# Optimization experiments

Hardware: AMD Instinct MI355X
Metric: run time of the kernel (lower is better)

Reference implementation:

```python
import jax, jax.numpy as jnp
import numpy as np

N_NODES = 50000
N_PATHS = 4
N_EDGES = 800000
D_IN = 256
D_OUT = 256
D_HID = 128  # SemanticAttention default hidden_size


def setup_inputs() -> dict:
    key = jax.random.key(0)
    ks = jax.random.split(key, 6)
    x = jax.random.normal(ks[0], (N_NODES, D_IN), dtype=jnp.float32)
    edge_indices = jax.random.randint(ks[1], (N_PATHS, 2, N_EDGES), 0, N_NODES)
    Ws = jax.random.normal(ks[2], (N_PATHS, D_IN, D_OUT), dtype=jnp.float32) * (1.0 / np.sqrt(D_IN))
    bs = jnp.zeros((N_PATHS, D_OUT), dtype=jnp.float32)
    attn_w1 = jax.random.normal(ks[3], (D_OUT, D_HID), dtype=jnp.float32) * (1.0 / np.sqrt(D_OUT))
    attn_b1 = jnp.zeros((D_HID,), dtype=jnp.float32)
    attn_w2 = jax.random.normal(ks[4], (D_HID, 1), dtype=jnp.float32) * (1.0 / np.sqrt(D_HID))
    return {"x": x, "edge_indices": edge_indices, "Ws": Ws, "bs": bs,
            "attn_w1": attn_w1, "attn_b1": attn_b1, "attn_w2": attn_w2}


def _gcn_conv(x, W, b, edges):
    """PyG GCNConv with normalize=True, add_self_loops=True.
    out = D^{-1/2} (A + I) D^{-1/2} (x @ W) + b
    """
    n = x.shape[0]
    xw = x @ W  # [N, D_OUT]
    loop = jnp.arange(n, dtype=edges.dtype)
    src = jnp.concatenate([edges[0], loop])
    dst = jnp.concatenate([edges[1], loop])
    ones = jnp.ones(src.shape[0], dtype=x.dtype)
    deg = jax.ops.segment_sum(ones, dst, num_segments=n)  # in-degree incl. self loop
    dinv = jnp.where(deg > 0, jax.lax.rsqrt(deg), 0.0)
    norm = dinv[src] * dinv[dst]  # [E+N]
    msgs = xw[src] * norm[:, None]  # gather + scale
    return jax.ops.segment_sum(msgs, dst, num_segments=n) + b  # scatter-add


def reference(x, edge_indices, Ws, bs, attn_w1, attn_b1, attn_w2):
    P = edge_indices.shape[0]
    # per-meta-path GCN embeddings, stacked -> [N, P, D_OUT]
    z = jnp.stack([_gcn_conv(x, Ws[i], bs[i], edge_indices[i]) for i in range(P)], axis=1)
    # semantic attention: per-node softmax over meta-paths
    w = jnp.tanh(z @ attn_w1 + attn_b1) @ attn_w2  # [N, P, 1]
    beta = jax.nn.softmax(w, axis=1)
    return (beta * z).sum(axis=1)  # [N, D_OUT]
```

## Files before the change

### kernel.cpp

```cpp
#include <hip/hip_runtime.h>
#include <hip/hip_fp16.h>
#include <cstdint>
#include <cstddef>

#define NN 50000
#define NE 800000
#define NP 4
#define DD 256
#define HH 128
#define MPAD 50048
#define PADIDX 50000
#define NCH 8

#define NB 196
#define CAP 5120
#define SCAP 6144
#define EPB 4096
#define NBB ((NE + EPB - 1) / EPB)
#define BIN_BLOCKS (NBB * NP)

typedef _Float16 f16x8 __attribute__((ext_vector_type(8)));
typedef float f32x4 __attribute__((ext_vector_type(4)));
typedef unsigned short u16x8 __attribute__((ext_vector_type(8)));

#define X_OCT (NN * DD / 8)
#define XP_OCT (MPAD * DD / 8)
#define W_OCT (NP * DD * DD / 8)
#define W1_OCT (HH * DD / 8)
#define CVT_BLOCKS ((XP_OCT + W_OCT + W1_OCT + 255) / 256)
#define AGG_BLOCKS (NCH * NP * (MPAD / 64))
#define GEMM_BLOCKS ((MPAD / 64) * NP)
#define AT_BLOCKS ((NN + 31) / 32)

__global__ __launch_bounds__(256) void k_bin(const int* __restrict__ edges,
                                             int* __restrict__ gcnt,
                                             unsigned int* __restrict__ binned,
                                             const float* __restrict__ x,
                                             const float* __restrict__ Ws,
                                             const float* __restrict__ w1,
                                             _Float16* __restrict__ xhc,
                                             _Float16* __restrict__ Wt,
                                             _Float16* __restrict__ w1t) {
    const int bx = blockIdx.x;
    const int tid = threadIdx.x;
    if (bx < BIN_BLOCKS) {
        __shared__ int hist[256], lb[256], cur[256], gbase[256], wsum[4];
        __shared__ unsigned int stage[EPB];
        const int p  = bx / NBB;
        const int bc = bx - p * NBB;
        const int e0 = bc * EPB;
        const int total = min(EPB, NE - e0);
        const int* es = edges + (size_t)p * 2 * NE;
        const int* ed = es + NE;
        hist[tid] = 0;
        __syncthreads();
        unsigned int word[16];
        int bkt[16];
#pragma unroll
        for (int j = 0; j < 16; j++) {
            int e = e0 + j * 256 + tid;
            bkt[j] = -1;
            if (e < NE) {
                int dst = ed[e];
                int src = es[e];
                int b = dst >> 8;
                bkt[j] = b;
                word[j] = ((unsigned)b << 24) | ((unsigned)(dst & 255) << 16) | (unsigned)src;
                atomicAdd(&hist[b], 1);
            }
        }
        __syncthreads();
        const int lane = tid & 63, wv = tid >> 6;
        int v = hist[tid];
        int incl = v;
#pragma unroll
        for (int off = 1; off < 64; off <<= 1) {
            int u = __shfl_up(incl, off);
            if (lane >= off) incl += u;
        }
        if (lane == 63) wsum[wv] = incl;
        __syncthreads();
        int wbase = 0;
        for (int i = 0; i < wv; i++) wbase += wsum[i];
        int excl = wbase + incl - v;
        lb[tid] = excl;
        cur[tid] = excl;
        if (tid < NB && v > 0) gbase[tid] = atomicAdd(&gcnt[p * NB + tid], v);
        __syncthreads();
#pragma unroll
        for (int j = 0; j < 16; j++)
            if (bkt[j] >= 0) {
                int r = atomicAdd(&cur[bkt[j]], 1);
                stage[r] = word[j];
            }
        __syncthreads();
        for (int s = tid; s < total; s += 256) {
            unsigned int wd = stage[s];
            int b = wd >> 24;
            int posl = gbase[b] + (s - lb[b]);
            if (posl < CAP)
                binned[(size_t)(p * NB + b) * CAP + posl] = wd & 0x00FFFFFFu;
        }
        return;
    }
    int i = (bx - BIN_BLOCKS) * 256 + tid;
    if (i < XP_OCT) {
        f16x8 o;
        if (i < X_OCT) {
            const float4* src = (const float4*)x + (size_t)i * 2;
            float4 v0 = src[0], v1 = src[1];
            o[0] = (_Float16)v0.x; o[1] = (_Float16)v0.y; o[2] = (_Float16)v0.z; o[3] = (_Float16)v0.w;
            o[4] = (_Float16)v1.x; o[5] = (_Float16)v1.y; o[6] = (_Float16)v1.z; o[7] = (_Float16)v1.w;
        } else {
#pragma unroll
            for (int t = 0; t < 8; t++) o[t] = (_Float16)0.0f;
        }
        int row = i >> 5, oc = i & 31;
        int c = oc >> 2, q = oc & 3;
        *(f16x8*)(xhc + ((size_t)c * MPAD + row) * 32 + q * 8) = o;
    } else if (i < XP_OCT + W_OCT) {
        int j = i - XP_OCT;
        int p   = j / (DD * DD / 8);
        int rem = j - p * (DD * DD / 8);
        int n   = rem >> 5;
        int k8  = (rem & 31) * 8;
        const float* wp = Ws + (size_t)p * DD * DD;
        f16x8 o;
#pragma unroll
        for (int t = 0; t < 8; t++) o[t] = (_Float16)wp[(size_t)(k8 + t) * DD + n];
        *((f16x8*)(Wt + (size_t)p * DD * DD + (size_t)n * DD + k8)) = o;
    } else if (i < XP_OCT + W_OCT + W1_OCT) {
        int j = i - XP_OCT - W_OCT;
        int n  = j >> 5;
        int k8 = (j & 31) * 8;
        f16x8 o;
#pragma unroll
        for (int t = 0; t < 8; t++) o[t] = (_Float16)w1[(size_t)(k8 + t) * HH + n];
        *((f16x8*)(w1t + (size_t)n * DD + k8)) = o;
    }
}

__global__ __launch_bounds__(256) void k_sort(const int* __restrict__ gcnt,
                                              const unsigned int* __restrict__ binned,
                                              unsigned short* __restrict__ srcs,
                                              int* __restrict__ offs,
                                              int* __restrict__ ends,
                                              float* __restrict__ dinv) {
    __shared__ int hist[256], cur[256], wsum[4];
    __shared__ unsigned short sorted[SCAP];
    const int bx = blockIdx.x;
    const int tid = threadIdx.x;
    const int p = bx / NB, b = bx - p * NB;
    const int base = bx * SCAP;
    const int n = min(gcnt[bx], CAP);
    hist[tid] = 0;
#pragma unroll
    for (int j = 0; j < SCAP / 256; j++) sorted[j * 256 + tid] = (unsigned short)PADIDX;
    __syncthreads();
    unsigned int w[20];
#pragma unroll
    for (int j = 0; j < 20; j++) {
        int s = j * 256 + tid;
        w[j] = 0xFFFFFFFFu;
        if (s < n) {
            w[j] = binned[(size_t)bx * CAP + s];
            atomicAdd(&hist[(w[j] >> 16) & 255], 1);
        }
    }
    __syncthreads();
    const int lane = tid & 63, wv = tid >> 6;
    int v  = hist[tid];
    int pv = (v + 7) & ~7;
    int incl = pv;
#pragma unroll
    for (int off = 1; off < 64; off <<= 1) {
        int u = __shfl_up(incl, off);
        if (lane >= off) incl += u;
    }
    if (lane == 63) wsum[wv] = incl;
    __syncthreads();
    int wbase = 0;
    for (int i = 0; i < wv; i++) wbase += wsum[i];
    int excl = wbase + incl - pv;
    cur[tid] = excl;
    const int node = b * 256 + tid;
    if (node < NN) {
        int o = base + excl;
        offs[p * NN + node] = o;
        ends[p * NN + node] = o + pv;
        dinv[(size_t)p * MPAD + node] = rsqrtf((float)v + 1.0f);
    }
    __syncthreads();
    int totalpad = wsum[0] + wsum[1] + wsum[2] + wsum[3];
#pragma unroll
    for (int j = 0; j < 20; j++)
        if (w[j] != 0xFFFFFFFFu) {
            int r = atomicAdd(&cur[(w[j] >> 16) & 255], 1);
            if (r < SCAP) sorted[r] = (unsigned short)(w[j] & 0xFFFFu);
        }
    __syncthreads();
#pragma unroll
    for (int j = 0; j < SCAP / 256; j++) {
        int s = j * 256 + tid;
        if (s < totalpad && s < SCAP) srcs[base + s] = sorted[s];
    }
}

__global__ __launch_bounds__(256) void k_agg(const _Float16* __restrict__ xhc,
                                             const float* __restrict__ dinv,
                                             const int* __restrict__ offs,
                                             const int* __restrict__ ends,
                                             const unsigned short* __restrict__ srcs,
                                             _Float16* __restrict__ aggc) {
    const int c  = blockIdx.x & 7;
    const int r  = blockIdx.x >> 3;
    const int p  = r / (MPAD / 64);
    const int nb = r - p * (MPAD / 64);
    const int wv = threadIdx.x >> 6;
    const int lane = threadIdx.x & 63;
    const int g = lane >> 2;
    const int f = lane & 3;
    const int n = nb * 64 + wv * 16 + g;

    const _Float16* xc = xhc + (size_t)c * MPAD * 32 + f * 8;
    const float* dvp = dinv + (size_t)p * MPAD;
    const float dd = dvp[n];

    float facc[8];
    {
        f16x8 xv = *(const f16x8*)(xc + (size_t)n * 32);
#pragma unroll
        for (int t = 0; t < 8; t++) facc[t] = dd * (float)xv[t];
    }
    if (n < NN) {
        int k  = offs[p * NN + n];
        int ke = ends[p * NN + n];
        for (; k < ke; k += 8) {
            u16x8 su = *(const u16x8*)(srcs + k);
            int s[8];
#pragma unroll
            for (int j = 0; j < 8; j++) s[j] = su[j];
            f16x8 v[8];
#pragma unroll
            for (int j = 0; j < 8; j++)
                v[j] = *(const f16x8*)(xc + (size_t)s[j] * 32);
            float dv[8];
#pragma unroll
            for (int j = 0; j < 8; j++) dv[j] = dvp[s[j]];
#pragma unroll
            for (int t = 0; t < 8; t++)
                facc[t] += ((dv[0] * (float)v[0][t] + dv[1] * (float)v[1][t]) +
                            (dv[2] * (float)v[2][t] + dv[3] * (float)v[3][t])) +
                           ((dv[4] * (float)v[4][t] + dv[5] * (float)v[5][t]) +
                            (dv[6] * (float)v[6][t] + dv[7] * (float)v[7][t]));
        }
    }
    f16x8 o;
#pragma unroll
    for (int t = 0; t < 8; t++) o[t] = (_Float16)(dd * facc[t]);
    *(f16x8*)(aggc + (((size_t)c * NP + p) * MPAD + n) * 32 + f * 8) = o;
}

__global__ __launch_bounds__(256) void k_gemm(const _Float16* __restrict__ aggc,
                                              const _Float16* __restrict__ Wt,
                                              const float* __restrict__ bs,
                                              _Float16* __restrict__ z) {
    const int gb   = blockIdx.x;
    const int p    = gb / (MPAD / 64);
    const int bm   = gb - p * (MPAD / 64);
    const int wv   = threadIdx.x >> 6;
    const int lane = threadIdx.x & 63;
    const int m_base = bm * 64;
    const int n0   = wv * 64;
    const int mr   = lane & 15;
    const int quad = lane >> 4;

    const _Float16* bp = Wt + (size_t)p * DD * DD + (size_t)(n0 + mr) * DD + quad * 8;
    _Float16* cp = z + (size_t)p * MPAD * DD;

    f32x4 acc[4][4] = {};
    for (int k0 = 0; k0 < DD; k0 += 32) {
        const int c = k0 >> 5;
        const _Float16* ap = aggc + (((size_t)c * NP + p) * MPAD + m_base + mr) * 32 + quad * 8;
        f16x8 a[4], b[4];
#pragma unroll
        for (int i = 0; i < 4; i++) a[i] = *(const f16x8*)(ap + (size_t)i * 16 * 32);
#pragma unroll
        for (int j = 0; j < 4; j++) b[j] = *(const f16x8*)(bp + (size_t)j * 16 * DD + k0);
#pragma unroll
        for (int i = 0; i < 4; i++)
#pragma unroll
            for (int j = 0; j < 4; j++)
                acc[i][j] = __builtin_amdgcn_mfma_f32_16x16x32_f16(a[i], b[j], acc[i][j], 0, 0, 0);
    }
    float bb[4];
#pragma unroll
    for (int j = 0; j < 4; j++) bb[j] = bs[p * DD + n0 + j * 16 + mr];
#pragma unroll
    for (int i = 0; i < 4; i++) {
#pragma unroll
        for (int r = 0; r < 4; r++) {
            int row = m_base + i * 16 + quad * 4 + r;
#pragma unroll
            for (int j = 0; j < 4; j++)
                cp[(size_t)row * DD + n0 + j * 16 + mr] = (_Float16)(acc[i][j][r] + bb[j]);
        }
    }
}

__global__ __launch_bounds__(512) void k_attn(const _Float16* __restrict__ z,
                                              const _Float16* __restrict__ w1t,
                                              const float* __restrict__ b1,
                                              const float* __restrict__ w2,
                                              float* __restrict__ out) {
    const int tid  = threadIdx.x;
    const int w    = tid >> 6;
    const int lane = tid & 63;
    const int quad = lane >> 4, mr = lane & 15;

    __shared__ __align__(16) _Float16 zs[128][264];

    const int nb = blockIdx.x * 32;

#pragma unroll
    for (int j = 0; j < 8; j++) {
        int o = j * 512 + tid;
        int r = o >> 5, oc = o & 31;
        int nl = r >> 2, p = r & 3;
        *(f16x8*)&zs[r][oc * 8] =
            *(const f16x8*)(z + ((size_t)p * MPAD + nb + nl) * DD + oc * 8);
    }
    __syncthreads();

    f32x4 acch[8] = {};
    for (int k0 = 0; k0 < DD; k0 += 32) {
        f16x8 a = *(const f16x8*)&zs[w * 16 + mr][k0 + quad * 8];
#pragma unroll
        for (int j = 0; j < 8; j++) {
            f16x8 b = *(const f16x8*)(w1t + (size_t)(j * 16 + mr) * DD + k0 + quad * 8);
            acch[j] = __builtin_amdgcn_mfma_f32_16x16x32_f16(a, b, acch[j], 0, 0, 0);
        }
    }

    float part[4] = {};
#pragma unroll
    for (int j = 0; j < 8; j++) {
        int col = j * 16 + mr;
        float bb = b1[col], ww = w2[col];
#pragma unroll
        for (int r = 0; r < 4; r++)
            part[r] += tanhf(acch[j][r] + bb) * ww;
    }
#pragma unroll
    for (int off = 1; off < 16; off <<= 1) {
#pragma unroll
        for (int r = 0; r < 4; r++) part[r] += __shfl_xor(part[r], off);
    }
    float m = fmaxf(fmaxf(part[0], part[1]), fmaxf(part[2], part[3]));
    float e0 = __expf(part[0] - m), e1 = __expf(part[1] - m),
          e2 = __expf(part[2] - m), e3 = __expf(part[3] - m);
    float rr = 1.0f / (e0 + e1 + e2 + e3);
    float be[4] = {e0 * rr, e1 * rr, e2 * rr, e3 * rr};

    const int n  = nb + w * 4 + quad;
    const int rb = w * 16 + quad * 4;
    float o[16] = {};
#pragma unroll
    for (int p = 0; p < 4; p++) {
        f16x8 z0 = *(const f16x8*)&zs[rb + p][mr * 16];
        f16x8 z1 = *(const f16x8*)&zs[rb + p][mr * 16 + 8];
#pragma unroll
        for (int t = 0; t < 8; t++) {
            o[t]     += be[p] * (float)z0[t];
            o[t + 8] += be[p] * (float)z1[t];
        }
    }
    if (n < NN) {
#pragma unroll
        for (int t = 0; t < 16; t += 4)
            *(float4*)(out + (size_t)n * DD + mr * 16 + t) =
                make_float4(o[t], o[t + 1], o[t + 2], o[t + 3]);
    }
}

extern "C" void kernel_launch(void* const* d_in, const int* in_sizes, int n_in,
                              void* d_out, int out_size, void* d_ws, size_t ws_size,
                              hipStream_t stream) {
    const float* x     = (const float*)d_in[0];
    const int*   edges = (const int*)d_in[1];
    const float* Ws    = (const float*)d_in[2];
    const float* bs    = (const float*)d_in[3];
    const float* w1    = (const float*)d_in[4];
    const float* b1    = (const float*)d_in[5];
    const float* w2    = (const float*)d_in[6];
    float* out = (float*)d_out;

    char* ws = (char*)d_ws;
    _Float16*       aggc   = (_Float16*)ws;
    _Float16*       Wt     = (_Float16*)(ws + (98 << 20));
    _Float16*       w1t    = (_Float16*)(ws + (98 << 20) + (1 << 19));
    _Float16*       z      = (_Float16*)(ws + (104 << 20));
    _Float16*       xhc    = (_Float16*)(ws + (104 << 20));
    unsigned int*   binned = (unsigned int*)(ws + (130 << 20));
    unsigned short* srcs   = (unsigned short*)(ws + (147 << 20));
    float*          dinv   = (float*)(ws + (157 << 20));
    int*            offs   = (int*)(ws + (158 << 20));
    int*            ends   = (int*)(ws + (159 << 20));
    int*            gcnt   = (int*)(ws + (160 << 20));

    hipMemsetAsync(gcnt, 0, NP * NB * sizeof(int), stream);
    hipMemsetAsync(dinv, 0, (size_t)NP * MPAD * sizeof(float), stream);

    k_bin<<<BIN_BLOCKS + CVT_BLOCKS, 256, 0, stream>>>(
        edges, gcnt, binned, x, Ws, w1, xhc, Wt, w1t);

    k_sort<<<NP * NB, 256, 0, stream>>>(gcnt, binned, srcs, offs, ends, dinv);

    k_agg<<<AGG_BLOCKS, 256, 0, stream>>>(xhc, dinv, offs, ends, srcs, aggc);

    k_gemm<<<GEMM_BLOCKS, 256, 0, stream>>>(aggc, Wt, bs, z);

    k_attn<<<AT_BLOCKS, 512, 0, stream>>>(z, w1t, b1, w2, out);
}
```

Before: 597.6 us.

## Degree-sort nodes per bin for balanced aggregation and precompute edge weights

Within each 256-node bin, nodes are reordered by padded in-degree and stored in slot arrays (node id, offset, degree), so threads in a wavefront handle nodes with similar edge counts and diverge less in the aggregation loop. A new kernel precomputes per-edge source dinv weights into a float array, replacing the dependent dinv gathers in k_agg with contiguous vector loads. This adds an extra launch, a 20MB weight array to write and read, and a second histogram/scan pass in k_sort.

```diff
diff --git a/kernel.cpp b/kernel.cpp
--- a/kernel.cpp
+++ b/kernel.cpp
@@ -18,6 +18,7 @@
 #define EPB 4096
 #define NBB ((NE + EPB - 1) / EPB)
 #define BIN_BLOCKS (NBB * NP)
+#define NSLOT (NB * 256)
 
 typedef _Float16 f16x8 __attribute__((ext_vector_type(8)));
 typedef float f32x4 __attribute__((ext_vector_type(4)));
@@ -28,9 +29,10 @@
 #define W_OCT (NP * DD * DD / 8)
 #define W1_OCT (HH * DD / 8)
 #define CVT_BLOCKS ((XP_OCT + W_OCT + W1_OCT + 255) / 256)
-#define AGG_BLOCKS (NCH * NP * (MPAD / 64))
+#define AGG_BLOCKS (NCH * NP * (NSLOT / 64))
 #define GEMM_BLOCKS ((MPAD / 64) * NP)
 #define AT_BLOCKS ((NN + 31) / 32)
+#define WT_BLOCKS (NP * NB * SCAP / 256)
 
 __global__ __launch_bounds__(256) void k_bin(const int* __restrict__ edges,
                                              int* __restrict__ gcnt,
@@ -143,9 +145,11 @@
 __global__ __launch_bounds__(256) void k_sort(const int* __restrict__ gcnt,
                                               const unsigned int* __restrict__ binned,
                                               unsigned short* __restrict__ srcs,
-                                              int* __restrict__ offs,
-                                              int* __restrict__ ends,
-                                              float* __restrict__ dinv) {
+                                              float* __restrict__ dinv,
+                                              unsigned short* __restrict__ nid,
+                                              int* __restrict__ offs2,
+                                              unsigned short* __restrict__ deg2)
+{
     __shared__ int hist[256], cur[256], wsum[4];
     __shared__ unsigned short sorted[SCAP];
     const int bx = blockIdx.x;
@@ -184,12 +188,8 @@
     int excl = wbase + incl - pv;
     cur[tid] = excl;
     const int node = b * 256 + tid;
-    if (node < NN) {
-        int o = base + excl;
-        offs[p * NN + node] = o;
-        ends[p * NN + node] = o + pv;
+    if (node < NN)
         dinv[(size_t)p * MPAD + node] = rsqrtf((float)v + 1.0f);
-    }
     __syncthreads();
     int totalpad = wsum[0] + wsum[1] + wsum[2] + wsum[3];
 #pragma unroll
@@ -204,61 +204,98 @@
         int s = j * 256 + tid;
         if (s < totalpad && s < SCAP) srcs[base + s] = sorted[s];
     }
+
+    __syncthreads();
+    hist[tid] = 0;
+    __syncthreads();
+    int key = min(pv >> 3, 255);
+    atomicAdd(&hist[key], 1);
+    __syncthreads();
+    int v2 = hist[tid];
+    int incl2 = v2;
+#pragma unroll
+    for (int off = 1; off < 64; off <<= 1) {
+        int u = __shfl_up(incl2, off);
+        if (lane >= off) incl2 += u;
+    }
+    if (lane == 63) wsum[wv] = incl2;
+    __syncthreads();
+    int wbase2 = 0;
+    for (int i = 0; i < wv; i++) wbase2 += wsum[i];
+    cur[tid] = wbase2 + incl2 - v2;
+    __syncthreads();
+    int slot = atomicAdd(&cur[key], 1);
+    int sbase = (p * NB + b) * 256;
+    nid[sbase + slot]   = (unsigned short)node;
+    offs2[sbase + slot] = base + excl;
+    deg2[sbase + slot]  = (unsigned short)pv;
+}
+
+__global__ __launch_bounds__(256) void k_wt(const unsigned short* __restrict__ srcs,
+                                            const float* __restrict__ dinv,
+                                            float* __restrict__ wts) {
+    int i = blockIdx.x * 256 + threadIdx.x;
+    int p = i / (NB * SCAP);
+    int s = min((int)srcs[i], MPAD - 1);
+    wts[i] = dinv[(size_t)p * MPAD + s];
 }
 
 __global__ __launch_bounds__(256) void k_agg(const _Float16* __restrict__ xhc,
                                              const float* __restrict__ dinv,
-                                             const int* __restrict__ offs,
-                                             const int* __restrict__ ends,
+                                             const unsigned short* __restrict__ nid,
+                                             const int* __restrict__ offs2,
+                                             const unsigned short* __restrict__ deg2,
                                              const unsigned short* __restrict__ srcs,
+                                             const float* __restrict__ wts,
                                              _Float16* __restrict__ aggc) {
     const int c  = blockIdx.x & 7;
     const int r  = blockIdx.x >> 3;
-    const int p  = r / (MPAD / 64);
-    const int nb = r - p * (MPAD / 64);
+    const int p  = r / (NSLOT / 64);
+    const int sb = (r - p * (NSLOT / 64)) * 64;
     const int wv = threadIdx.x >> 6;
     const int lane = threadIdx.x & 63;
     const int g = lane >> 2;
     const int f = lane & 3;
-    const int n = nb * 64 + wv * 16 + g;
+    const int slot = p * NSLOT + sb + wv * 16 + g;
+
+    const int n  = nid[slot];
+    const int o  = offs2[slot];
+    const int pv = deg2[slot];
 
     const _Float16* xc = xhc + (size_t)c * MPAD * 32 + f * 8;
-    const float* dvp = dinv + (size_t)p * MPAD;
-    const float dd = dvp[n];
-
-    float facc[8];
-    {
+    const float dd = (n < NN) ? dinv[(size_t)p * MPAD + n] : 0.0f;
+
+    float facc[8] = {};
+    if (n < MPAD) {
         f16x8 xv = *(const f16x8*)(xc + (size_t)n * 32);
 #pragma unroll
         for (int t = 0; t < 8; t++) facc[t] = dd * (float)xv[t];
     }
-    if (n < NN) {
-        int k  = offs[p * NN + n];
-        int ke = ends[p * NN + n];
-        for (; k < ke; k += 8) {
-            u16x8 su = *(const u16x8*)(srcs + k);
-            int s[8];
-#pragma unroll
-            for (int j = 0; j < 8; j++) s[j] = su[j];
-            f16x8 v[8];
-#pragma unroll
-            for (int j = 0; j < 8; j++)
-                v[j] = *(const f16x8*)(xc + (size_t)s[j] * 32);
-            float dv[8];
-#pragma unroll
-            for (int j = 0; j < 8; j++) dv[j] = dvp[s[j]];
-#pragma unroll
-            for (int t = 0; t < 8; t++)
-                facc[t] += ((dv[0] * (float)v[0][t] + dv[1] * (float)v[1][t]) +
-                            (dv[2] * (float)v[2][t] + dv[3] * (float)v[3][t])) +
-                           ((dv[4] * (float)v[4][t] + dv[5] * (float)v[5][t]) +
-                            (dv[6] * (float)v[6][t] + dv[7] * (float)v[7][t]));
-        }
-    }
-    f16x8 o;
-#pragma unroll
-    for (int t = 0; t < 8; t++) o[t] = (_Float16)(dd * facc[t]);
-    *(f16x8*)(aggc + (((size_t)c * NP + p) * MPAD + n) * 32 + f * 8) = o;
+    for (int k = o; k < o + pv; k += 8) {
+        u16x8 su = *(const u16x8*)(srcs + k);
+        float4 wa = *(const float4*)(wts + k);
+        float4 wb = *(const float4*)(wts + k + 4);
+        int s[8];
+#pragma unroll
+        for (int j = 0; j < 8; j++) s[j] = su[j];
+        f16x8 v[8];
+#pragma unroll
+        for (int j = 0; j < 8; j++)
+            v[j] = *(const f16x8*)(xc + (size_t)s[j] * 32);
+        float w[8] = {wa.x, wa.y, wa.z, wa.w, wb.x, wb.y, wb.z, wb.w};
+#pragma unroll
+        for (int t = 0; t < 8; t++)
+            facc[t] += ((w[0] * (float)v[0][t] + w[1] * (float)v[1][t]) +
+                        (w[2] * (float)v[2][t] + w[3] * (float)v[3][t])) +
+                       ((w[4] * (float)v[4][t] + w[5] * (float)v[5][t]) +
+                        (w[6] * (float)v[6][t] + w[7] * (float)v[7][t]));
+    }
+    if (n < MPAD) {
+        f16x8 ot;
+#pragma unroll
+        for (int t = 0; t < 8; t++) ot[t] = (_Float16)(dd * facc[t]);
+        *(f16x8*)(aggc + (((size_t)c * NP + p) * MPAD + n) * 32 + f * 8) = ot;
+    }
 }
 
 __global__ __launch_bounds__(256) void k_gemm(const _Float16* __restrict__ aggc,
@@ -403,10 +440,12 @@
     _Float16*       xhc    = (_Float16*)(ws + (104 << 20));
     unsigned int*   binned = (unsigned int*)(ws + (130 << 20));
     unsigned short* srcs   = (unsigned short*)(ws + (147 << 20));
-    float*          dinv   = (float*)(ws + (157 << 20));
-    int*            offs   = (int*)(ws + (158 << 20));
-    int*            ends   = (int*)(ws + (159 << 20));
-    int*            gcnt   = (int*)(ws + (160 << 20));
+    float*          wts    = (float*)(ws + (157 << 20));
+    float*          dinv   = (float*)(ws + (177 << 20));
+    unsigned short* nid    = (unsigned short*)(ws + (178 << 20));
+    int*            offs2  = (int*)(ws + (179 << 20));
+    unsigned short* deg2   = (unsigned short*)(ws + (180 << 20));
+    int*            gcnt   = (int*)(ws + (181 << 20));
 
     hipMemsetAsync(gcnt, 0, NP * NB * sizeof(int), stream);
     hipMemsetAsync(dinv, 0, (size_t)NP * MPAD * sizeof(float), stream);
@@ -414,9 +453,11 @@
     k_bin<<<BIN_BLOCKS + CVT_BLOCKS, 256, 0, stream>>>(
         edges, gcnt, binned, x, Ws, w1, xhc, Wt, w1t);
 
-    k_sort<<<NP * NB, 256, 0, stream>>>(gcnt, binned, srcs, offs, ends, dinv);
-
-    k_agg<<<AGG_BLOCKS, 256, 0, stream>>>(xhc, dinv, offs, ends, srcs, aggc);
+    k_sort<<<NP * NB, 256, 0, stream>>>(gcnt, binned, srcs, dinv, nid, offs2, deg2);
+
+    k_wt<<<WT_BLOCKS, 256, 0, stream>>>(srcs, dinv, wts);
+
+    k_agg<<<AGG_BLOCKS, 256, 0, stream>>>(xhc, dinv, nid, offs2, deg2, srcs, wts, aggc);
 
     k_gemm<<<GEMM_BLOCKS, 256, 0, stream>>>(aggc, Wt, bs, z);
 
```

After: 602.1 us. No clear change (+0.8%).

## Aggregate full feature rows per half-wave with fp16 packed accumulation

Applied to the files above, without the earlier changes.

Drops the 8-way channel-chunked layout of x and the aggregate, and uses plain row-major fp16 rows instead. Each half-wave now gathers one whole 512-byte neighbour row, so the edge list and index loads are read once per node rather than once per chunk. Accumulation moves to packed fp16 vector FMAs split across two accumulators, with an fp16 copy of dinv for the neighbour weights. This cuts index traffic and ALU work but loses precision, since sums of up to dozens of neighbours are now held in fp16.

```diff
diff --git a/kernel.cpp b/kernel.cpp
--- a/kernel.cpp
+++ b/kernel.cpp
@@ -10,7 +10,6 @@
 #define HH 128
 #define MPAD 50048
 #define PADIDX 50000
-#define NCH 8
 
 #define NB 196
 #define CAP 5120
@@ -28,7 +27,7 @@
 #define W_OCT (NP * DD * DD / 8)
 #define W1_OCT (HH * DD / 8)
 #define CVT_BLOCKS ((XP_OCT + W_OCT + W1_OCT + 255) / 256)
-#define AGG_BLOCKS (NCH * NP * (MPAD / 64))
+#define AGG_BLOCKS (NP * (MPAD / 8))
 #define GEMM_BLOCKS ((MPAD / 64) * NP)
 #define AT_BLOCKS ((NN + 31) / 32)
 
@@ -38,7 +37,7 @@
                                              const float* __restrict__ x,
                                              const float* __restrict__ Ws,
                                              const float* __restrict__ w1,
-                                             _Float16* __restrict__ xhc,
+                                             _Float16* __restrict__ xh,
                                              _Float16* __restrict__ Wt,
                                              _Float16* __restrict__ w1t) {
     const int bx = blockIdx.x;
@@ -115,9 +114,7 @@
 #pragma unroll
             for (int t = 0; t < 8; t++) o[t] = (_Float16)0.0f;
         }
-        int row = i >> 5, oc = i & 31;
-        int c = oc >> 2, q = oc & 3;
-        *(f16x8*)(xhc + ((size_t)c * MPAD + row) * 32 + q * 8) = o;
+        *((f16x8*)xh + i) = o;
     } else if (i < XP_OCT + W_OCT) {
         int j = i - XP_OCT;
         int p   = j / (DD * DD / 8);
@@ -145,7 +142,8 @@
                                               unsigned short* __restrict__ srcs,
                                               int* __restrict__ offs,
                                               int* __restrict__ ends,
-                                              float* __restrict__ dinv) {
+                                              float* __restrict__ dinv,
+                                              _Float16* __restrict__ dinvh) {
     __shared__ int hist[256], cur[256], wsum[4];
     __shared__ unsigned short sorted[SCAP];
     const int bx = blockIdx.x;
@@ -188,7 +186,9 @@
         int o = base + excl;
         offs[p * NN + node] = o;
         ends[p * NN + node] = o + pv;
-        dinv[(size_t)p * MPAD + node] = rsqrtf((float)v + 1.0f);
+        float dv = rsqrtf((float)v + 1.0f);
+        dinv[(size_t)p * MPAD + node]  = dv;
+        dinvh[(size_t)p * MPAD + node] = (_Float16)dv;
     }
     __syncthreads();
     int totalpad = wsum[0] + wsum[1] + wsum[2] + wsum[3];
@@ -206,32 +206,29 @@
     }
 }
 
-__global__ __launch_bounds__(256) void k_agg(const _Float16* __restrict__ xhc,
+__global__ __launch_bounds__(256) void k_agg(const _Float16* __restrict__ xh,
                                              const float* __restrict__ dinv,
+                                             const _Float16* __restrict__ dinvh,
                                              const int* __restrict__ offs,
                                              const int* __restrict__ ends,
                                              const unsigned short* __restrict__ srcs,
-                                             _Float16* __restrict__ aggc) {
-    const int c  = blockIdx.x & 7;
-    const int r  = blockIdx.x >> 3;
-    const int p  = r / (MPAD / 64);
-    const int nb = r - p * (MPAD / 64);
-    const int wv = threadIdx.x >> 6;
+                                             _Float16* __restrict__ agg) {
+    const int bxp = blockIdx.x;
+    const int p   = bxp / (MPAD / 8);
+    const int bm  = bxp - p * (MPAD / 8);
+    const int wv  = threadIdx.x >> 6;
     const int lane = threadIdx.x & 63;
-    const int g = lane >> 2;
-    const int f = lane & 3;
-    const int n = nb * 64 + wv * 16 + g;
-
-    const _Float16* xc = xhc + (size_t)c * MPAD * 32 + f * 8;
-    const float* dvp = dinv + (size_t)p * MPAD;
-    const float dd = dvp[n];
-
-    float facc[8];
-    {
-        f16x8 xv = *(const f16x8*)(xc + (size_t)n * 32);
-#pragma unroll
-        for (int t = 0; t < 8; t++) facc[t] = dd * (float)xv[t];
-    }
+    const int hl  = lane & 31;
+    const int n   = bm * 8 + wv * 2 + (lane >> 5);
+
+    const float dd = dinv[(size_t)p * MPAD + n];
+    const _Float16* dvh = dinvh + (size_t)p * MPAD;
+    const _Float16 ddh = (_Float16)dd;
+
+    f16x8 xv = *(const f16x8*)(xh + (size_t)n * DD + hl * 8);
+    f16x8 acc0 = xv * ddh;
+    f16x8 acc1 = {};
+
     if (n < NN) {
         int k  = offs[p * NN + n];
         int ke = ends[p * NN + n];
@@ -240,28 +237,27 @@
             int s[8];
 #pragma unroll
             for (int j = 0; j < 8; j++) s[j] = su[j];
+            _Float16 wh[8];
+#pragma unroll
+            for (int j = 0; j < 8; j++) wh[j] = dvh[s[j]];
             f16x8 v[8];
 #pragma unroll
             for (int j = 0; j < 8; j++)
-                v[j] = *(const f16x8*)(xc + (size_t)s[j] * 32);
-            float dv[8];
-#pragma unroll
-            for (int j = 0; j < 8; j++) dv[j] = dvp[s[j]];
-#pragma unroll
-            for (int t = 0; t < 8; t++)
-                facc[t] += ((dv[0] * (float)v[0][t] + dv[1] * (float)v[1][t]) +
-                            (dv[2] * (float)v[2][t] + dv[3] * (float)v[3][t])) +
-                           ((dv[4] * (float)v[4][t] + dv[5] * (float)v[5][t]) +
-                            (dv[6] * (float)v[6][t] + dv[7] * (float)v[7][t]));
+                v[j] = *(const f16x8*)(xh + (size_t)s[j] * DD + hl * 8);
+            acc0 += v[0] * wh[0]; acc1 += v[1] * wh[1];
+            acc0 += v[2] * wh[2]; acc1 += v[3] * wh[3];
+            acc0 += v[4] * wh[4]; acc1 += v[5] * wh[5];
+            acc0 += v[6] * wh[6]; acc1 += v[7] * wh[7];
         }
     }
     f16x8 o;
 #pragma unroll
-    for (int t = 0; t < 8; t++) o[t] = (_Float16)(dd * facc[t]);
-    *(f16x8*)(aggc + (((size_t)c * NP + p) * MPAD + n) * 32 + f * 8) = o;
-}
-
-__global__ __launch_bounds__(256) void k_gemm(const _Float16* __restrict__ aggc,
+    for (int t = 0; t < 8; t++)
+        o[t] = (_Float16)(dd * ((float)acc0[t] + (float)acc1[t]));
+    *(f16x8*)(agg + ((size_t)p * MPAD + n) * DD + hl * 8) = o;
+}
+
+__global__ __launch_bounds__(256) void k_gemm(const _Float16* __restrict__ agg,
                                               const _Float16* __restrict__ Wt,
                                               const float* __restrict__ bs,
                                               _Float16* __restrict__ z) {
@@ -275,16 +271,15 @@
     const int mr   = lane & 15;
     const int quad = lane >> 4;
 
+    const _Float16* ap = agg + ((size_t)p * MPAD + m_base + mr) * DD + quad * 8;
     const _Float16* bp = Wt + (size_t)p * DD * DD + (size_t)(n0 + mr) * DD + quad * 8;
     _Float16* cp = z + (size_t)p * MPAD * DD;
 
     f32x4 acc[4][4] = {};
     for (int k0 = 0; k0 < DD; k0 += 32) {
-        const int c = k0 >> 5;
-        const _Float16* ap = aggc + (((size_t)c * NP + p) * MPAD + m_base + mr) * 32 + quad * 8;
         f16x8 a[4], b[4];
 #pragma unroll
-        for (int i = 0; i < 4; i++) a[i] = *(const f16x8*)(ap + (size_t)i * 16 * 32);
+        for (int i = 0; i < 4; i++) a[i] = *(const f16x8*)(ap + (size_t)i * 16 * DD + k0);
 #pragma unroll
         for (int j = 0; j < 4; j++) b[j] = *(const f16x8*)(bp + (size_t)j * 16 * DD + k0);
 #pragma unroll
@@ -396,29 +391,31 @@
     float* out = (float*)d_out;
 
     char* ws = (char*)d_ws;
-    _Float16*       aggc   = (_Float16*)ws;
+    _Float16*       agg    = (_Float16*)ws;
     _Float16*       Wt     = (_Float16*)(ws + (98 << 20));
     _Float16*       w1t    = (_Float16*)(ws + (98 << 20) + (1 << 19));
     _Float16*       z      = (_Float16*)(ws + (104 << 20));
-    _Float16*       xhc    = (_Float16*)(ws + (104 << 20));
+    _Float16*       xh     = (_Float16*)(ws + (104 << 20));
     unsigned int*   binned = (unsigned int*)(ws + (130 << 20));
     unsigned short* srcs   = (unsigned short*)(ws + (147 << 20));
     float*          dinv   = (float*)(ws + (157 << 20));
-    int*            offs   = (int*)(ws + (158 << 20));
-    int*            ends   = (int*)(ws + (159 << 20));
-    int*            gcnt   = (int*)(ws + (160 << 20));
+    _Float16*       dinvh  = (_Float16*)(ws + (158 << 20));
+    int*            offs   = (int*)(ws + (159 << 20));
+    int*            ends   = (int*)(ws + (160 << 20));
+    int*            gcnt   = (int*)(ws + (161 << 20));
 
     hipMemsetAsync(gcnt, 0, NP * NB * sizeof(int), stream);
     hipMemsetAsync(dinv, 0, (size_t)NP * MPAD * sizeof(float), stream);
+    hipMemsetAsync(dinvh, 0, (size_t)NP * MPAD * sizeof(_Float16), stream);
 
     k_bin<<<BIN_BLOCKS + CVT_BLOCKS, 256, 0, stream>>>(
-        edges, gcnt, binned, x, Ws, w1, xhc, Wt, w1t);
-
-    k_sort<<<NP * NB, 256, 0, stream>>>(gcnt, binned, srcs, offs, ends, dinv);
-
-    k_agg<<<AGG_BLOCKS, 256, 0, stream>>>(xhc, dinv, offs, ends, srcs, aggc);
-
-    k_gemm<<<GEMM_BLOCKS, 256, 0, stream>>>(aggc, Wt, bs, z);
+        edges, gcnt, binned, x, Ws, w1, xh, Wt, w1t);
+
+    k_sort<<<NP * NB, 256, 0, stream>>>(gcnt, binned, srcs, offs, ends, dinv, dinvh);
+
+    k_agg<<<AGG_BLOCKS, 256, 0, stream>>>(xh, dinv, dinvh, offs, ends, srcs, agg);
+
+    k_gemm<<<GEMM_BLOCKS, 256, 0, stream>>>(agg, Wt, bs, z);
 
     k_attn<<<AT_BLOCKS, 512, 0, stream>>>(z, w1t, b1, w2, out);
 }
```

After: 602.2 us. Within noise of the previous version (+0.8%).
